# Kernel tuning notes

Measured on AMD Instinct MI355X. Metric: run time of the kernel, lower is better.

Reference implementation:

```python
import jax, jax.numpy as jnp
import numpy as np

NEG_SLOPE = 0.2  # PyG GATConv default
BN_EPS = 1e-5
NUM_GRAPHS = 128


def _bn(x, g, b, m, v):
    # eval-mode BatchNorm1d with running stats
    return (x - m) * jax.lax.rsqrt(v + BN_EPS) * g + b


def _gat_conv(x, src, dst, mask, W, a_src, a_dst, bias):
    # PyG GATConv: per-head linear, edge logits LeakyReLU(a_src.Wx_j + a_dst.Wx_i),
    # segment-softmax over incoming edges of each dst node, scatter-add messages.
    N = x.shape[0]
    H, C = a_src.shape
    xw = (x @ W).reshape(N, H, C)                       # [N,H,C]
    logit_s = (xw * a_src).sum(-1)                      # [N,H]
    logit_d = (xw * a_dst).sum(-1)                      # [N,H]
    e = jax.nn.leaky_relu(logit_s[src] + logit_d[dst], NEG_SLOPE)  # [E,H]
    e = jnp.where(mask[:, None], e, -1e30)              # edges filtered by edge_weights==1
    m = jax.ops.segment_max(e, dst, num_segments=N)     # [N,H]
    m = jnp.maximum(m, -1e30)                           # guard empty segments
    p = jnp.exp(e - m[dst]) * mask[:, None].astype(e.dtype)
    denom = jax.ops.segment_sum(p, dst, num_segments=N) + 1e-16
    alpha = p / denom[dst]                              # [E,H]
    out = jax.ops.segment_sum(xw[src] * alpha[..., None], dst, num_segments=N)
    return out.reshape(N, H * C) + bias


def setup_inputs() -> dict:
    key = jax.random.key(0)
    ks = jax.random.split(key, 20)
    N, E, F, G, NC = 20000, 320000, 128, NUM_GRAPHS, 10
    E0, E1, H = 256, 512, 2
    C = E1 // H

    def lin(k, fi, fo):
        return jax.random.normal(k, (fi, fo), jnp.float32) / np.float32(np.sqrt(fi))

    def bn(k, n):
        k1, k2, k3, k4 = jax.random.split(k, 4)
        g = 1.0 + 0.1 * jax.random.normal(k1, (n,), jnp.float32)
        b = 0.1 * jax.random.normal(k2, (n,), jnp.float32)
        m = 0.1 * jax.random.normal(k3, (n,), jnp.float32)
        v = 1.0 + 0.5 * jax.random.uniform(k4, (n,), jnp.float32)
        return g, b, m, v

    d = {}
    d['x'] = jax.random.normal(ks[0], (N, F), jnp.float32)
    d['edge_index'] = jax.random.randint(ks[1], (2, E), 0, N, dtype=jnp.int32)
    d['edge_weights'] = jnp.ones((E,), jnp.int32)
    d['batch'] = jnp.sort(jax.random.randint(ks[2], (N,), 0, G, dtype=jnp.int32))
    d['mlp_w1'] = lin(ks[3], F, E0); d['mlp_b1'] = jnp.zeros((E0,), jnp.float32)
    d['bn1_g'], d['bn1_b'], d['bn1_m'], d['bn1_v'] = bn(ks[4], E0)
    d['mlp_w2'] = lin(ks[5], E0, E0); d['mlp_b2'] = jnp.zeros((E0,), jnp.float32)
    d['bn2_g'], d['bn2_b'], d['bn2_m'], d['bn2_v'] = bn(ks[6], E0)
    d['gat0_w'] = lin(ks[7], E0, H * C)
    d['gat0_asrc'] = 0.1 * jax.random.normal(ks[8], (H, C), jnp.float32)
    d['gat0_adst'] = 0.1 * jax.random.normal(ks[9], (H, C), jnp.float32)
    d['gat0_bias'] = jnp.zeros((H * C,), jnp.float32)
    d['gat1_w'] = lin(ks[10], E1, H * C)
    d['gat1_asrc'] = 0.1 * jax.random.normal(ks[11], (H, C), jnp.float32)
    d['gat1_adst'] = 0.1 * jax.random.normal(ks[12], (H, C), jnp.float32)
    d['gat1_bias'] = jnp.zeros((H * C,), jnp.float32)
    d['bn3_g'], d['bn3_b'], d['bn3_m'], d['bn3_v'] = bn(ks[13], E1)
    d['fin_w1'] = lin(ks[14], E1, E1); d['fin_b1'] = jnp.zeros((E1,), jnp.float32)
    d['fin_w2'] = lin(ks[15], E1, NC); d['fin_b2'] = jnp.zeros((NC,), jnp.float32)
    return d


def reference(x, edge_index, edge_weights, batch,
              mlp_w1, mlp_b1, bn1_g, bn1_b, bn1_m, bn1_v,
              mlp_w2, mlp_b2, bn2_g, bn2_b, bn2_m, bn2_v,
              gat0_w, gat0_asrc, gat0_adst, gat0_bias,
              gat1_w, gat1_asrc, gat1_adst, gat1_bias,
              bn3_g, bn3_b, bn3_m, bn3_v,
              fin_w1, fin_b1, fin_w2, fin_b2):
    src, dst = edge_index[0], edge_index[1]
    mask = edge_weights == 1
    # initial MLP (dropout is identity in eval)
    h = jax.nn.relu(_bn(x @ mlp_w1 + mlp_b1, bn1_g, bn1_b, bn1_m, bn1_v))
    h = jax.nn.relu(_bn(h @ mlp_w2 + mlp_b2, bn2_g, bn2_b, bn2_m, bn2_v))
    # GAT layers
    h = _gat_conv(h, src, dst, mask, gat0_w, gat0_asrc, gat0_adst, gat0_bias)
    h = _gat_conv(h, src, dst, mask, gat1_w, gat1_asrc, gat1_adst, gat1_bias)
    # global mean pool over graphs
    sums = jax.ops.segment_sum(h, batch, num_segments=NUM_GRAPHS)
    cnt = jax.ops.segment_sum(jnp.ones((h.shape[0], 1), h.dtype), batch, num_segments=NUM_GRAPHS)
    pooled = sums / jnp.maximum(cnt, 1.0)
    # final head: BN -> ReLU -> Linear -> ReLU -> Linear
    z = jax.nn.relu(_bn(pooled, bn3_g, bn3_b, bn3_m, bn3_v))
    z = jax.nn.relu(z @ fin_w1 + fin_b1)
    return z @ fin_w2 + fin_b2
```

## Files before the change

kernel.cpp:

```cpp
#include <hip/hip_runtime.h>

typedef unsigned short u16;

constexpr int NN = 20000;
constexpr int EE = 320000;
constexpr int FD = 128;
constexpr int C0 = 256;
constexpr int C1 = 512;
constexpr int NG = 128;
constexpr int NC = 10;
constexpr int NBLK = (NN + 255) / 256;
constexpr int HB  = 320;
constexpr int EST = HB * 256;
constexpr int LGB = 640;
constexpr int PSPL = 16;

constexpr size_t OFF_XB   = 0;
constexpr size_t OFF_H1   = OFF_XB  + (size_t)NN * FD * 2;
constexpr size_t OFF_H2   = OFF_H1  + (size_t)NN * C0 * 2;
constexpr size_t OFF_XW   = OFF_H2  + (size_t)NN * C0 * 2;
constexpr size_t OFF_H34  = OFF_XW  + (size_t)NN * C1 * 2;
constexpr size_t OFF_LS   = OFF_H34 + (size_t)NN * C1 * 2;
constexpr size_t OFF_LD   = OFF_LS  + (size_t)NN * 2 * 4;
constexpr size_t OFF_DEG  = OFF_LD  + (size_t)NN * 2 * 4;
constexpr size_t OFF_OFFS = OFF_DEG + (size_t)NN * 4;
constexpr size_t OFF_CUR  = OFF_OFFS + 80016;
constexpr size_t OFF_CSRC = OFF_CUR + (size_t)NN * 4;
constexpr size_t OFF_GCNT = OFF_CSRC + (size_t)EE * 4;
constexpr size_t OFF_GOFF = OFF_GCNT + 512;
constexpr size_t OFF_PART = OFF_GOFF + 768;
constexpr size_t OFF_PTOT = OFF_PART + 512;
constexpr size_t OFF_Z1   = OFF_PTOT + 256;
constexpr size_t OFF_Z2   = OFF_Z1  + (size_t)NG * C1 * 2;
constexpr size_t OFF_ST   = OFF_Z2  + (size_t)NG * C1 * 2;
constexpr size_t OFF_W1T  = OFF_ST  + 8192;
constexpr size_t OFF_W2T  = OFF_W1T + (size_t)FD * C0 * 2;
constexpr size_t OFF_G0T  = OFF_W2T + (size_t)C0 * C0 * 2;
constexpr size_t OFF_G1T  = OFF_G0T + (size_t)C0 * C1 * 2;
constexpr size_t OFF_AUX  = OFF_G1T + (size_t)C1 * C1 * 2;
constexpr size_t OFF_FLAG = OFF_AUX  + 0;
constexpr size_t OFF_A0S  = OFF_AUX  + 256;
constexpr size_t OFF_A0D  = OFF_AUX  + 1280;
constexpr size_t OFF_A1S  = OFF_AUX  + 2304;
constexpr size_t OFF_A1D  = OFF_AUX  + 3328;
constexpr size_t OFF_GB0  = OFF_AUX  + 4352;
constexpr size_t OFF_GB1  = OFF_AUX  + 6400;
constexpr size_t OFF_FB1  = OFF_AUX  + 8448;
constexpr size_t OFF_FB2  = OFF_AUX  + 10496;
constexpr size_t OFF_GMX  = OFF_AUX  + 10752;
constexpr size_t OFF_PP   = OFF_AUX  + 11008;
constexpr size_t OFF_DENA = OFF_PP + (size_t)NG * PSPL * C1 * 4;
constexpr size_t OFF_P0   = OFF_XB;
constexpr size_t OFF_P1   = OFF_XB + (size_t)EE * 4;

__device__ inline float bf2f(u16 u) { return __uint_as_float(((unsigned)u) << 16); }
__device__ inline u16 f2bf(float f) {
    unsigned u = __float_as_uint(f);
    unsigned r = u + 0x7fffu + ((u >> 16) & 1u);
    return (u16)(r >> 16);
}
__device__ inline float ldf(const void* p, long i, unsigned f) {
    return f ? ((const float*)p)[i] : bf2f(((const u16*)p)[i]);
}
__device__ inline unsigned encf(float f) {
    unsigned u = __float_as_uint(f);
    return (u & 0x80000000u) ? ~u : (u | 0x80000000u);
}
__device__ inline float decf(unsigned e) {
    return (e & 0x80000000u) ? __uint_as_float(e ^ 0x80000000u) : __uint_as_float(~e);
}
__device__ inline void unpack8(uint4 r, float* v) {
    v[0] = __uint_as_float(r.x << 16); v[1] = __uint_as_float(r.x & 0xffff0000u);
    v[2] = __uint_as_float(r.y << 16); v[3] = __uint_as_float(r.y & 0xffff0000u);
    v[4] = __uint_as_float(r.z << 16); v[5] = __uint_as_float(r.z & 0xffff0000u);
    v[6] = __uint_as_float(r.w << 16); v[7] = __uint_as_float(r.w & 0xffff0000u);
}

typedef __bf16 bf16x8_t __attribute__((ext_vector_type(8)));
typedef float  f32x4_t  __attribute__((ext_vector_type(4)));

__device__ __forceinline__ void gl_lds16(const u16* g, u16* l) {
    __builtin_amdgcn_global_load_lds((const __attribute__((address_space(1))) void*)g,
                                     (__attribute__((address_space(3))) void*)l, 16, 0, 0);
}

__global__ void detect_dtype(const u16* __restrict__ x, const u16* __restrict__ w,
                             const u16* __restrict__ fw, unsigned* flag) {
    __shared__ int cnt;
    if (threadIdx.x == 0) cnt = 0;
    __syncthreads();
    int c = 0;
    for (int i = threadIdx.x; i < 4096; i += 256) {
        c += (((x[i]  >> 7) & 0xFF) == 0xFF);
        c += (((w[i]  >> 7) & 0xFF) == 0xFF);
        c += (((fw[i] >> 7) & 0xFF) == 0xFF);
    }
    atomicAdd(&cnt, c);
    __syncthreads();
    if (threadIdx.x == 0) *flag = (cnt >= 2) ? 1u : 0u;
}

__global__ void cvt_x(const unsigned* __restrict__ flag, const void* __restrict__ xin,
                      u16* __restrict__ XB, int* __restrict__ deg, int* __restrict__ gcnt,
                      unsigned* __restrict__ gmxu) {
    int i = blockIdx.x * 256 + threadIdx.x;
    if (i < NN) deg[i] = 0;
    if (i < NG) gcnt[i] = 0;
    if (i < 4)  gmxu[i] = encf(-1e30f);
    if (*flag) {
        float4 v = ((const float4*)xin)[i];
        ushort4 r;
        r.x = f2bf(v.x); r.y = f2bf(v.y); r.z = f2bf(v.z); r.w = f2bf(v.w);
        ((ushort4*)XB)[i] = r;
    } else {
        ((ushort4*)XB)[i] = ((const ushort4*)xin)[i];
    }
}

__global__ __launch_bounds__(512) void prep_trans(const unsigned* __restrict__ flag,
                            const void* g1, const void* b1, const void* m1, const void* v1, const void* lb1,
                            const void* g2, const void* b2, const void* m2, const void* v2, const void* lb2,
                            const void* g3, const void* b3, const void* m3, const void* v3,
                            const void* a0s, const void* a0d, const void* gb0in,
                            const void* a1s, const void* a1d, const void* gb1in,
                            const void* fb1in, const void* fb2in,
                            float* S1, float* T1, float* S2, float* T2, float* S3, float* T3,
                            u16* A0S, u16* A0D, u16* A1S, u16* A1D,
                            float* GB0, float* GB1, float* FB1, float* FB2,
                            const void* w1, const void* w2, const void* g0w, const void* g1w,
                            u16* w1T, u16* w2T, u16* g0T, u16* g1T) {
    unsigned f = *flag;
    if (blockIdx.x == 0) {
        int c = threadIdx.x;
        if (c < 256) {
            float s = ldf(g1, c, f) / sqrtf(ldf(v1, c, f) + 1e-5f);
            S1[c] = s; T1[c] = s * (ldf(lb1, c, f) - ldf(m1, c, f)) + ldf(b1, c, f);
            float s2 = ldf(g2, c, f) / sqrtf(ldf(v2, c, f) + 1e-5f);
            S2[c] = s2; T2[c] = s2 * (ldf(lb2, c, f) - ldf(m2, c, f)) + ldf(b2, c, f);
        }
        float s3 = ldf(g3, c, f) / sqrtf(ldf(v3, c, f) + 1e-5f);
        S3[c] = s3; T3[c] = ldf(b3, c, f) - ldf(m3, c, f) * s3;
        A0S[c] = f2bf(ldf(a0s, c, f));
        A0D[c] = f2bf(ldf(a0d, c, f));
        A1S[c] = f2bf(ldf(a1s, c, f));
        A1D[c] = f2bf(ldf(a1d, c, f));
        GB0[c] = ldf(gb0in, c, f);
        GB1[c] = ldf(gb1in, c, f);
        FB1[c] = ldf(fb1in, c, f);
        if (c < NC) FB2[c] = ldf(fb2in, c, f);
        return;
    }
    int b = blockIdx.x - 1;
    const void* B; u16* BT; int K, logN, base;
    if (b < 64)       { B = w1;  BT = w1T; K = FD; logN = 8; base = 0; }
    else if (b < 192) { B = w2;  BT = w2T; K = C0; logN = 8; base = 64; }
    else if (b < 448) { B = g0w; BT = g0T; K = C0; logN = 9; base = 192; }
    else              { B = g1w; BT = g1T; K = C1; logN = 9; base = 448; }
    int idx = (b - base) * 512 + threadIdx.x;
    int N = 1 << logN;
    int k = idx >> logN, n = idx & (N - 1);
    u16 v = f ? f2bf(((const float*)B)[idx]) : ((const u16*)B)[idx];
    BT[(size_t)n * K + k] = v;
}

__global__ __launch_bounds__(256) void hist_k(const int* __restrict__ dst, const int* __restrict__ ew,
                                              const int* __restrict__ batch,
                                              int* __restrict__ deg, int* __restrict__ gcnt) {
    int tid = blockIdx.x * 256 + threadIdx.x;
    int lane = threadIdx.x & 63;
#pragma unroll
    for (int j = 0; j < 4; j++) {
        int e = tid + j * EST;
        if (e < EE && ew[e] == 1) atomicAdd(&deg[dst[e]], 1);
    }
    int n = tid;
    if (n < NN) {
        int g = batch[n];
        int pg = __shfl_up(g, 1);
        bool head = (lane == 0) || (pg != g);
        unsigned long long act = __ballot(1);
        unsigned long long hm  = __ballot(head);
        if (head) {
            unsigned long long above = (lane < 63) ? ((hm >> (lane + 1)) << (lane + 1)) : 0ull;
            int limit = 64 - __builtin_clzll(act);
            int nxt = above ? __builtin_ctzll(above) : limit;
            atomicAdd(&gcnt[g], nxt - lane);
        }
    }
}
__global__ __launch_bounds__(256) void scan_blk(const int* __restrict__ deg, int* __restrict__ off,
                                                int* __restrict__ part) {
    __shared__ int tmp[256];
    int tid = threadIdx.x, i = blockIdx.x * 256 + tid;
    int v = (i < NN) ? deg[i] : 0;
    tmp[tid] = v;
    __syncthreads();
#pragma unroll
    for (int s = 1; s < 256; s <<= 1) {
        int a = (tid >= s) ? tmp[tid - s] : 0;
        __syncthreads();
        if (tid >= s) tmp[tid] += a;
        __syncthreads();
    }
    if (i < NN) off[i] = tmp[tid] - v;
    if (tid == 255) part[blockIdx.x] = tmp[255];
}
__global__ __launch_bounds__(128) void scan_small(int* __restrict__ part, int* __restrict__ ptot,
                                                  const int* __restrict__ gcnt, int* __restrict__ goff) {
    __shared__ int tmp[128];
    int tid = threadIdx.x;
    int v = (tid < NBLK) ? part[tid] : 0;
    tmp[tid] = v;
    __syncthreads();
#pragma unroll
    for (int s = 1; s < 128; s <<= 1) {
        int a = (tid >= s) ? tmp[tid - s] : 0;
        __syncthreads();
        if (tid >= s) tmp[tid] += a;
        __syncthreads();
    }
    if (tid < NBLK) part[tid] = tmp[tid] - v;
    if (tid == 127) *ptot = tmp[127];
    __syncthreads();
    int g = gcnt[tid];
    tmp[tid] = g;
    __syncthreads();
#pragma unroll
    for (int s = 1; s < 128; s <<= 1) {
        int a = (tid >= s) ? tmp[tid - s] : 0;
        __syncthreads();
        if (tid >= s) tmp[tid] += a;
        __syncthreads();
    }
    goff[tid] = tmp[tid] - g;
    if (tid == 127) goff[128] = tmp[127];
}
__global__ __launch_bounds__(256) void scan_add(int* __restrict__ off, const int* __restrict__ part,
                                                const int* __restrict__ ptot, int* __restrict__ cursor) {
    int tid = threadIdx.x, i = blockIdx.x * 256 + tid;
    if (i < NN) {
        int o = off[i] + part[blockIdx.x];
        off[i] = o;
        cursor[i] = o;
    }
    if (i == 0) off[NN] = *ptot;
}
__global__ __launch_bounds__(256) void csr_fill(const int* __restrict__ src, const int* __restrict__ dst,
                                                const int* __restrict__ ew,
                                                int* __restrict__ cursor, u16* __restrict__ csrc) {
    int tid = blockIdx.x * 256 + threadIdx.x;
    bool ok[4]; int sv[4]; int p[4];
#pragma unroll
    for (int j = 0; j < 4; j++) {
        int e = tid + j * EST;
        ok[j] = false; sv[j] = 0; p[j] = 0;
        if (e < EE && ew[e] == 1) {
            ok[j] = true;
            sv[j] = src[e];
            p[j] = atomicAdd(&cursor[dst[e]], 1);
        }
    }
#pragma unroll
    for (int j = 0; j < 4; j++) if (ok[j]) csrc[p[j]] = (u16)sv[j];
}

template <int EPI>
__global__ __launch_bounds__(256) void gemm_tile(const u16* __restrict__ A, const u16* __restrict__ BT,
                                                 u16* __restrict__ Cm,
                                                 const float* __restrict__ S, const float* __restrict__ T,
                                                 int M, int N, int K) {
    __shared__ u16 As[128 * 32];
    __shared__ u16 Bs[128 * 32];
    const int tid  = threadIdx.x;
    const int wave = tid >> 6;
    const int lane = tid & 63;
    const int quad = lane >> 4;
    const int l16  = lane & 15;
    const int wr0  = (wave >> 1) * 64;
    const int wc0  = (wave & 1) * 64;
    const int row0 = blockIdx.x * 128;
    const int col0 = blockIdx.y * 128;

    const int lr = lane >> 2;
    const int lk = (lane & 3) * 8;
    int r0l = wave * 32 + lr;
    int r1l = r0l + 16;
    int gr0 = row0 + r0l; if (gr0 >= M) gr0 = M - 1;
    int gr1 = row0 + r1l; if (gr1 >= M) gr1 = M - 1;
    const u16* ga0 = A  + (size_t)gr0 * K + lk;
    const u16* ga1 = A  + (size_t)gr1 * K + lk;
    const u16* gb0 = BT + (size_t)(col0 + r0l) * K + lk;
    const u16* gb1 = BT + (size_t)(col0 + r1l) * K + lk;
    u16* la0 = As + (size_t)(wave * 32)      * 32 + lane * 8;
    u16* la1 = As + (size_t)(wave * 32 + 16) * 32 + lane * 8;
    u16* lb0 = Bs + (size_t)(wave * 32)      * 32 + lane * 8;
    u16* lb1 = Bs + (size_t)(wave * 32 + 16) * 32 + lane * 8;

    f32x4_t acc[4][4];
#pragma unroll
    for (int r = 0; r < 4; r++)
#pragma unroll
        for (int c = 0; c < 4; c++)
#pragma unroll
            for (int i = 0; i < 4; i++) acc[r][c][i] = 0.f;

    for (int k0 = 0; k0 < K; k0 += 32) {
        gl_lds16(ga0 + k0, la0);
        gl_lds16(ga1 + k0, la1);
        gl_lds16(gb0 + k0, lb0);
        gl_lds16(gb1 + k0, lb1);
        __syncthreads();

        bf16x8_t a[4], b[4];
#pragma unroll
        for (int r = 0; r < 4; r++)
            a[r] = *(const bf16x8_t*)(As + (size_t)(wr0 + r * 16 + l16) * 32 + quad * 8);
#pragma unroll
        for (int c = 0; c < 4; c++)
            b[c] = *(const bf16x8_t*)(Bs + (size_t)(wc0 + c * 16 + l16) * 32 + quad * 8);
#pragma unroll
        for (int r = 0; r < 4; r++)
#pragma unroll
            for (int c = 0; c < 4; c++)
                acc[r][c] = __builtin_amdgcn_mfma_f32_16x16x32_bf16(a[r], b[c], acc[r][c], 0, 0, 0);
        __syncthreads();
    }

#pragma unroll
    for (int r = 0; r < 4; r++) {
        int rb = row0 + wr0 + r * 16 + quad * 4;
#pragma unroll
        for (int c = 0; c < 4; c++) {
            int col = col0 + wc0 + c * 16 + l16;
            float sc = (EPI == 1) ? S[col] : 0.f;
            float sh = (EPI == 1) ? T[col] : 0.f;
#pragma unroll
            for (int i = 0; i < 4; i++) {
                int row = rb + i;
                if (row < M) {
                    float v = acc[r][c][i];
                    if (EPI == 1) v = fmaxf(v * sc + sh, 0.f);
                    Cm[(size_t)row * N + col] = f2bf(v);
                }
            }
        }
    }
}

__global__ __launch_bounds__(256) void gat_logits(const u16* __restrict__ xw, const u16* __restrict__ asrc,
                                                  const u16* __restrict__ adst, float* __restrict__ ls,
                                                  float* __restrict__ ld, unsigned* __restrict__ gmx) {
    __shared__ float smax[8];
    int lane = threadIdx.x & 63;
    int wv   = threadIdx.x >> 6;
    int h    = lane >> 5;
    uint4 av = ((const uint4*)asrc)[lane];
    uint4 dv = ((const uint4*)adst)[lane];
    float a[8], d[8];
    unpack8(av, a); unpack8(dv, d);
    float mm = -1e30f;
    int n = blockIdx.x * 4 + wv;
    uint4 xv;
    if (n < NN) xv = ((const uint4*)(xw + (size_t)n * C1))[lane];
    while (n < NN) {
        int n2 = n + LGB * 4;
        uint4 nx;
        if (n2 < NN) nx = ((const uint4*)(xw + (size_t)n2 * C1))[lane];
        float x[8];
        unpack8(xv, x);
        float ps = 0.f, pd = 0.f;
#pragma unroll
        for (int j = 0; j < 8; j++) { ps += x[j] * a[j]; pd += x[j] * d[j]; }
#pragma unroll
        for (int m = 16; m >= 1; m >>= 1) { ps += __shfl_xor(ps, m); pd += __shfl_xor(pd, m); }
        if ((lane & 31) == 0) {
            ls[n * 2 + h] = ps;
            ld[n * 2 + h] = pd;
        }
        mm = fmaxf(mm, ps);
        xv = nx; n = n2;
    }
    if ((lane & 31) == 0) smax[wv * 2 + h] = mm;
    __syncthreads();
    if (threadIdx.x < 2) {
        float m = fmaxf(fmaxf(smax[threadIdx.x], smax[2 + threadIdx.x]),
                        fmaxf(smax[4 + threadIdx.x], smax[6 + threadIdx.x]));
        atomicMax(&gmx[threadIdx.x], encf(m));
    }
}

__global__ __launch_bounds__(256) void gat_prep(const int* __restrict__ off, const u16* __restrict__ csrc,
                                                const float* __restrict__ ls, const float* __restrict__ ld,
                                                const unsigned* __restrict__ gmx,
                                                float* __restrict__ P0, float* __restrict__ P1,
                                                float* __restrict__ denA) {
    int n = blockIdx.x * 4 + (threadIdx.x >> 6);
    if (n >= NN) return;
    int lane = threadIdx.x & 63;
    int h = lane >> 5;
    int el = lane & 31;
    int beg = off[n], end = off[n + 1];
    float2 ldv = ((const float2*)ld)[n];
    float ldh = h ? ldv.y : ldv.x;
    float gm = decf(gmx[h]) + ldh;
    float mhat = gm > 0.f ? gm : 0.2f * gm;
    float* __restrict__ Ph = h ? P1 : P0;
    float den = 0.f;
    for (int base = beg; base < end; base += 32) {
        int e = base + el;
        int ec = e < end ? e : end - 1;
        int sv = csrc[ec];
        float vv = ls[sv * 2 + h] + ldh;
        vv = vv > 0.f ? vv : 0.2f * vv;
        float p = __expf(vv - mhat);
        float pm = (e < end) ? p : 0.f;
#pragma unroll
        for (int m = 16; m >= 1; m >>= 1) pm += __shfl_xor(pm, m);
        den += pm;
        if (e < end) Ph[e] = p;
    }
    if (el == 0) denA[n * 2 + h] = den;
}

__device__ __forceinline__ void proc_edge(uint4 c, float w, float* acc) {
    float x[8];
    unpack8(c, x);
#pragma unroll
    for (int q = 0; q < 8; q++) acc[q] = fmaf(w, x[q], acc[q]);
}

__global__ __launch_bounds__(256) void gat_aggregate(const int* __restrict__ off, const u16* __restrict__ csrc,
                                                     const float* __restrict__ P0, const float* __restrict__ P1,
                                                     const float* __restrict__ denA,
                                                     const u16* __restrict__ xw,
                                                     const float* __restrict__ bias, u16* __restrict__ outh) {
    int n = blockIdx.x * 4 + (threadIdx.x >> 6);
    if (n >= NN) return;
    const int lane = threadIdx.x & 63;
    const int h    = lane >> 5;
    const int el   = lane & 31;
    const int hoff = h << 5;
    const float* __restrict__ Ph = h ? P1 : P0;
    int beg = off[n], end = off[n + 1];

    float acc[8];
#pragma unroll
    for (int q = 0; q < 8; q++) acc[q] = 0.f;

#define ROWLD(S) (((const uint4*)(xw + (size_t)(S) * C1))[lane])

    for (int base = beg; base < end; base += 32) {
        int cnt = end - base; if (cnt > 32) cnt = 32;
        int e = base + el;
        int ec = e < end ? e : end - 1;
        int sv = csrc[ec];
        float pv = Ph[ec];

        uint4 r0 = ROWLD(__shfl(sv, 0));
        uint4 r1 = ROWLD(__shfl(sv, 1));
        uint4 r2 = ROWLD(__shfl(sv, 2));
        uint4 r3 = ROWLD(__shfl(sv, 3));

        for (int j = 0; j < cnt; j += 4) {
            uint4 c0 = r0, c1 = r1, c2 = r2, c3 = r3;
            float w0 = __shfl(pv, j + hoff);
            float w1 = __shfl(pv, j + 1 + hoff);
            float w2 = __shfl(pv, j + 2 + hoff);
            float w3 = __shfl(pv, j + 3 + hoff);
            if (j + 4 < cnt) {
                r0 = ROWLD(__shfl(sv, j + 4));
                r1 = ROWLD(__shfl(sv, j + 5));
                r2 = ROWLD(__shfl(sv, j + 6));
                r3 = ROWLD(__shfl(sv, j + 7));
            }
            proc_edge(c0, w0, acc);
            if (j + 1 < cnt) proc_edge(c1, w1, acc);
            if (j + 2 < cnt) proc_edge(c2, w2, acc);
            if (j + 3 < cnt) proc_edge(c3, w3, acc);
        }
    }
#undef ROWLD

    float inv = 1.f / fmaxf(denA[n * 2 + h], 1e-30f);
    int cb = lane * 8;
    const float4* bp = (const float4*)(bias + cb);
    float4 b0 = bp[0], b1 = bp[1];
    uint4 st;
    st.x = (unsigned)f2bf(fmaf(acc[0], inv, b0.x)) | ((unsigned)f2bf(fmaf(acc[1], inv, b0.y)) << 16);
    st.y = (unsigned)f2bf(fmaf(acc[2], inv, b0.z)) | ((unsigned)f2bf(fmaf(acc[3], inv, b0.w)) << 16);
    st.z = (unsigned)f2bf(fmaf(acc[4], inv, b1.x)) | ((unsigned)f2bf(fmaf(acc[5], inv, b1.y)) << 16);
    st.w = (unsigned)f2bf(fmaf(acc[6], inv, b1.z)) | ((unsigned)f2bf(fmaf(acc[7], inv, b1.w)) << 16);
    ((uint4*)(outh + (size_t)n * C1 + cb))[0] = st;
}

__global__ __launch_bounds__(128) void pool_part(const u16* __restrict__ h4, const int* __restrict__ goff,
                                                 float* __restrict__ pp) {
    int g = blockIdx.x, s = blockIdx.y, t = threadIdx.x;
    int b = goff[g], e = goff[g + 1];
    int len = e - b;
    int chunk = (len + PSPL - 1) / PSPL;
    int n0 = b + s * chunk;
    int n1 = n0 + chunk; if (n1 > e) n1 = e;
    float s0 = 0.f, s1 = 0.f, s2 = 0.f, s3 = 0.f;
    for (int n = n0; n < n1; n++) {
        ushort4 v = *(const ushort4*)(h4 + (size_t)n * C1 + t * 4);
        s0 += bf2f(v.x); s1 += bf2f(v.y); s2 += bf2f(v.z); s3 += bf2f(v.w);
    }
    float4* dst = (float4*)(pp + ((size_t)g * PSPL + s) * C1 + t * 4);
    *dst = make_float4(s0, s1, s2, s3);
}

__global__ __launch_bounds__(512) void head_all(const unsigned* __restrict__ flag,
                                                const float* __restrict__ pp, const int* __restrict__ goff,
                                                const float* __restrict__ S3, const float* __restrict__ T3,
                                                const void* __restrict__ w1, const float* __restrict__ FB1,
                                                const void* __restrict__ w2, const float* __restrict__ FB2,
                                                void* __restrict__ out) {
    __shared__ float zrow[512];
    __shared__ float z2row[512];
    __shared__ float red[512];
    int g = blockIdx.x, t = threadIdx.x;
    unsigned f = *flag;
    float s = 0.f;
#pragma unroll
    for (int k = 0; k < PSPL; k++) s += pp[((size_t)g * PSPL + k) * C1 + t];
    int b = goff[g], e = goff[g + 1];
    float mean = s / fmaxf((float)(e - b), 1.f);
    float v = fmaxf(mean * S3[t] + T3[t], 0.f);
    zrow[t] = bf2f(f2bf(v));
    __syncthreads();
    float acc = 0.f;
    if (f) {
        const float* w = (const float*)w1;
        for (int k = 0; k < 512; k++) acc = fmaf(zrow[k], w[(size_t)k * 512 + t], acc);
    } else {
        const u16* w = (const u16*)w1;
        for (int k = 0; k < 512; k++) acc = fmaf(zrow[k], bf2f(w[(size_t)k * 512 + t]), acc);
    }
    acc += FB1[t];
    z2row[t] = bf2f(f2bf(fmaxf(acc, 0.f)));
    __syncthreads();
    float z2t = z2row[t];
    for (int o = 0; o < NC; o++) {
        float p = f ? z2t * ((const float*)w2)[(size_t)t * NC + o]
                    : z2t * bf2f(((const u16*)w2)[(size_t)t * NC + o]);
        red[t] = p;
        __syncthreads();
#pragma unroll
        for (int sd = 256; sd >= 1; sd >>= 1) {
            if (t < sd) red[t] += red[t + sd];
            __syncthreads();
        }
        if (t == 0) {
            float vv = red[0] + FB2[o];
            if (f) ((float*)out)[g * NC + o] = vv;
            else   ((u16*)out)[g * NC + o] = f2bf(vv);
        }
        __syncthreads();
    }
}

extern "C" void kernel_launch(void* const* d_in, const int* in_sizes, int n_in,
                              void* d_out, int out_size, void* d_ws, size_t ws_size,
                              hipStream_t stream) {
    (void)in_sizes; (void)n_in; (void)out_size; (void)ws_size;

    const void* x      = d_in[0];
    const int* ei      = (const int*)d_in[1];
    const int* src     = ei;
    const int* dst     = ei + EE;
    const int* ew      = (const int*)d_in[2];
    const int* batch   = (const int*)d_in[3];
    const void* mlp_w1 = d_in[4];
    const void* mlp_b1 = d_in[5];
    const void *bn1g = d_in[6], *bn1b = d_in[7], *bn1m = d_in[8], *bn1v = d_in[9];
    const void* mlp_w2 = d_in[10];
    const void* mlp_b2 = d_in[11];
    const void *bn2g = d_in[12], *bn2b = d_in[13], *bn2m = d_in[14], *bn2v = d_in[15];
    const void* g0w    = d_in[16];
    const void* g0as   = d_in[17];
    const void* g0ad   = d_in[18];
    const void* g0bias = d_in[19];
    const void* g1w    = d_in[20];
    const void* g1as   = d_in[21];
    const void* g1ad   = d_in[22];
    const void* g1bias = d_in[23];
    const void *bn3g = d_in[24], *bn3b = d_in[25], *bn3m = d_in[26], *bn3v = d_in[27];
    const void* fin_w1 = d_in[28];
    const void* fin_b1 = d_in[29];
    const void* fin_w2 = d_in[30];
    const void* fin_b2 = d_in[31];

    char* ws = (char*)d_ws;
    u16*  XB   = (u16*)(ws + OFF_XB);
    u16*  h1   = (u16*)(ws + OFF_H1);
    u16*  h2   = (u16*)(ws + OFF_H2);
    u16*  xw   = (u16*)(ws + OFF_XW);
    u16*  h34  = (u16*)(ws + OFF_H34);
    float* ls  = (float*)(ws + OFF_LS);
    float* ld  = (float*)(ws + OFF_LD);
    int*  deg  = (int*)(ws + OFF_DEG);
    int*  off  = (int*)(ws + OFF_OFFS);
    int*  cur  = (int*)(ws + OFF_CUR);
    u16*  csrc = (u16*)(ws + OFF_CSRC);
    int*  gcnt = (int*)(ws + OFF_GCNT);
    int*  goff = (int*)(ws + OFF_GOFF);
    int*  part = (int*)(ws + OFF_PART);
    int*  ptot = (int*)(ws + OFF_PTOT);
    float* S1 = (float*)(ws + OFF_ST);
    float* T1 = S1 + 256;
    float* S2 = T1 + 256;
    float* T2 = S2 + 256;
    float* S3 = T2 + 256;
    float* T3 = S3 + 512;
    u16* w1T = (u16*)(ws + OFF_W1T);
    u16* w2T = (u16*)(ws + OFF_W2T);
    u16* g0T = (u16*)(ws + OFF_G0T);
    u16* g1T = (u16*)(ws + OFF_G1T);
    unsigned* flag = (unsigned*)(ws + OFF_FLAG);
    u16* A0S = (u16*)(ws + OFF_A0S);
    u16* A0D = (u16*)(ws + OFF_A0D);
    u16* A1S = (u16*)(ws + OFF_A1S);
    u16* A1D = (u16*)(ws + OFF_A1D);
    float* GB0 = (float*)(ws + OFF_GB0);
    float* GB1 = (float*)(ws + OFF_GB1);
    float* FB1 = (float*)(ws + OFF_FB1);
    float* FB2 = (float*)(ws + OFF_FB2);
    unsigned* GMXU = (unsigned*)(ws + OFF_GMX);
    float* PP = (float*)(ws + OFF_PP);
    float* DENA = (float*)(ws + OFF_DENA);
    float* P0 = (float*)(ws + OFF_P0);
    float* P1 = (float*)(ws + OFF_P1);

    detect_dtype<<<1, 256, 0, stream>>>((const u16*)x, (const u16*)mlp_w1, (const u16*)fin_w1, flag);
    cvt_x<<<(NN * FD / 4) / 256, 256, 0, stream>>>(flag, x, XB, deg, gcnt, GMXU);
    prep_trans<<<961, 512, 0, stream>>>(flag,
                                        bn1g, bn1b, bn1m, bn1v, mlp_b1,
                                        bn2g, bn2b, bn2m, bn2v, mlp_b2,
                                        bn3g, bn3b, bn3m, bn3v,
                                        g0as, g0ad, g0bias, g1as, g1ad, g1bias,
                                        fin_b1, fin_b2,
                                        S1, T1, S2, T2, S3, T3,
                                        A0S, A0D, A1S, A1D, GB0, GB1, FB1, FB2,
                                        mlp_w1, mlp_w2, g0w, g1w, w1T, w2T, g0T, g1T);

    hist_k<<<HB, 256, 0, stream>>>(dst, ew, batch, deg, gcnt);
    scan_blk<<<NBLK, 256, 0, stream>>>(deg, off, part);
    scan_small<<<1, 128, 0, stream>>>(part, ptot, gcnt, goff);
    scan_add<<<NBLK, 256, 0, stream>>>(off, part, ptot, cur);
    csr_fill<<<HB, 256, 0, stream>>>(src, dst, ew, cur, csrc);

    gemm_tile<1><<<dim3(157, 2), 256, 0, stream>>>(XB, w1T, h1, S1, T1, NN, C0, FD);
    gemm_tile<1><<<dim3(157, 2), 256, 0, stream>>>(h1, w2T, h2, S2, T2, NN, C0, C0);

    gemm_tile<0><<<dim3(157, 4), 256, 0, stream>>>(h2, g0T, xw, nullptr, nullptr, NN, C1, C0);
    gat_logits<<<LGB, 256, 0, stream>>>(xw, A0S, A0D, ls, ld, GMXU);
    gat_prep<<<NN / 4, 256, 0, stream>>>(off, csrc, ls, ld, GMXU, P0, P1, DENA);
    gat_aggregate<<<NN / 4, 256, 0, stream>>>(off, csrc, P0, P1, DENA, xw, GB0, h34);

    gemm_tile<0><<<dim3(157, 4), 256, 0, stream>>>(h34, g1T, xw, nullptr, nullptr, NN, C1, C1);
    gat_logits<<<LGB, 256, 0, stream>>>(xw, A1S, A1D, ls, ld, GMXU + 2);
    gat_prep<<<NN / 4, 256, 0, stream>>>(off, csrc, ls, ld, GMXU + 2, P0, P1, DENA);
    gat_aggregate<<<NN / 4, 256, 0, stream>>>(off, csrc, P0, P1, DENA, xw, GB1, h34);

    pool_part<<<dim3(NG, PSPL), 128, 0, stream>>>(h34, goff, PP);
    head_all<<<NG, 512, 0, stream>>>(flag, PP, goff, S3, T3, fin_w1, FB1, fin_w2, FB2, d_out);
}
```

Before: 405.7 us.

## Fuse GAT logit dot-products into GEMM epilogue and use exact per-node max

The attention logit projections (xw·a_src, xw·a_dst) are now computed in the GEMM epilogue from the rounded outputs. Partial sums per column tile go to a buffer, and a small ls_combine kernel adds them. This removes the separate gat_logits pass that re-read xw, and it drops the global-max atomic and its init. gat_prep now makes an extra pass over each node's edges to compute the exact per-segment max instead of a global upper bound. Separately, the GEMM K-step doubles to 64 with an XOR-swizzled LDS layout, which means fewer barriers but more shared memory per block.

```diff
diff --git a/kernel.cpp b/kernel.cpp
--- a/kernel.cpp
+++ b/kernel.cpp
@@ -12,7 +12,6 @@
 constexpr int NBLK = (NN + 255) / 256;
 constexpr int HB  = 320;
 constexpr int EST = HB * 256;
-constexpr int LGB = 640;
 constexpr int PSPL = 16;
 
 constexpr size_t OFF_XB   = 0;
@@ -47,9 +46,9 @@
 constexpr size_t OFF_GB1  = OFF_AUX  + 6400;
 constexpr size_t OFF_FB1  = OFF_AUX  + 8448;
 constexpr size_t OFF_FB2  = OFF_AUX  + 10496;
-constexpr size_t OFF_GMX  = OFF_AUX  + 10752;
 constexpr size_t OFF_PP   = OFF_AUX  + 11008;
 constexpr size_t OFF_DENA = OFF_PP + (size_t)NG * PSPL * C1 * 4;
+constexpr size_t OFF_PLS  = OFF_DENA + (size_t)NN * 2 * 4;
 constexpr size_t OFF_P0   = OFF_XB;
 constexpr size_t OFF_P1   = OFF_XB + (size_t)EE * 4;
 
@@ -62,13 +61,6 @@
 __device__ inline float ldf(const void* p, long i, unsigned f) {
     return f ? ((const float*)p)[i] : bf2f(((const u16*)p)[i]);
 }
-__device__ inline unsigned encf(float f) {
-    unsigned u = __float_as_uint(f);
-    return (u & 0x80000000u) ? ~u : (u | 0x80000000u);
-}
-__device__ inline float decf(unsigned e) {
-    return (e & 0x80000000u) ? __uint_as_float(e ^ 0x80000000u) : __uint_as_float(~e);
-}
 __device__ inline void unpack8(uint4 r, float* v) {
     v[0] = __uint_as_float(r.x << 16); v[1] = __uint_as_float(r.x & 0xffff0000u);
     v[2] = __uint_as_float(r.y << 16); v[3] = __uint_as_float(r.y & 0xffff0000u);
@@ -101,12 +93,10 @@
 }
 
 __global__ void cvt_x(const unsigned* __restrict__ flag, const void* __restrict__ xin,
-                      u16* __restrict__ XB, int* __restrict__ deg, int* __restrict__ gcnt,
-                      unsigned* __restrict__ gmxu) {
+                      u16* __restrict__ XB, int* __restrict__ deg, int* __restrict__ gcnt) {
     int i = blockIdx.x * 256 + threadIdx.x;
     if (i < NN) deg[i] = 0;
     if (i < NG) gcnt[i] = 0;
-    if (i < 4)  gmxu[i] = encf(-1e30f);
     if (*flag) {
         float4 v = ((const float4*)xin)[i];
         ushort4 r;
@@ -268,9 +258,11 @@
 __global__ __launch_bounds__(256) void gemm_tile(const u16* __restrict__ A, const u16* __restrict__ BT,
                                                  u16* __restrict__ Cm,
                                                  const float* __restrict__ S, const float* __restrict__ T,
+                                                 const u16* __restrict__ asrc, const u16* __restrict__ adst,
+                                                 float2* __restrict__ pls,
                                                  int M, int N, int K) {
-    __shared__ u16 As[128 * 32];
-    __shared__ u16 Bs[128 * 32];
+    __shared__ u16 As[128 * 64];
+    __shared__ u16 Bs[128 * 64];
     const int tid  = threadIdx.x;
     const int wave = tid >> 6;
     const int lane = tid & 63;
@@ -281,20 +273,18 @@
     const int row0 = blockIdx.x * 128;
     const int col0 = blockIdx.y * 128;
 
-    const int lr = lane >> 2;
-    const int lk = (lane & 3) * 8;
-    int r0l = wave * 32 + lr;
-    int r1l = r0l + 16;
-    int gr0 = row0 + r0l; if (gr0 >= M) gr0 = M - 1;
-    int gr1 = row0 + r1l; if (gr1 >= M) gr1 = M - 1;
-    const u16* ga0 = A  + (size_t)gr0 * K + lk;
-    const u16* ga1 = A  + (size_t)gr1 * K + lk;
-    const u16* gb0 = BT + (size_t)(col0 + r0l) * K + lk;
-    const u16* gb1 = BT + (size_t)(col0 + r1l) * K + lk;
-    u16* la0 = As + (size_t)(wave * 32)      * 32 + lane * 8;
-    u16* la1 = As + (size_t)(wave * 32 + 16) * 32 + lane * 8;
-    u16* lb0 = Bs + (size_t)(wave * 32)      * 32 + lane * 8;
-    u16* lb1 = Bs + (size_t)(wave * 32 + 16) * 32 + lane * 8;
+    const int srow = lane >> 3;
+    const int sk   = ((lane & 7) ^ srow) * 8;
+    const u16* gaP[4]; const u16* gbP[4]; u16* laP[4]; u16* lbP[4];
+#pragma unroll
+    for (int i = 0; i < 4; i++) {
+        int rl = wave * 32 + i * 8 + srow;
+        int gr = row0 + rl; if (gr >= M) gr = M - 1;
+        gaP[i] = A  + (size_t)gr * K + sk;
+        gbP[i] = BT + (size_t)(col0 + rl) * K + sk;
+        laP[i] = As + (size_t)rl * 64 + (lane & 7) * 8;
+        lbP[i] = Bs + (size_t)rl * 64 + (lane & 7) * 8;
+    }
 
     f32x4_t acc[4][4];
 #pragma unroll
@@ -304,94 +294,107 @@
 #pragma unroll
             for (int i = 0; i < 4; i++) acc[r][c][i] = 0.f;
 
-    for (int k0 = 0; k0 < K; k0 += 32) {
-        gl_lds16(ga0 + k0, la0);
-        gl_lds16(ga1 + k0, la1);
-        gl_lds16(gb0 + k0, lb0);
-        gl_lds16(gb1 + k0, lb1);
-        __syncthreads();
-
-        bf16x8_t a[4], b[4];
-#pragma unroll
-        for (int r = 0; r < 4; r++)
-            a[r] = *(const bf16x8_t*)(As + (size_t)(wr0 + r * 16 + l16) * 32 + quad * 8);
-#pragma unroll
-        for (int c = 0; c < 4; c++)
-            b[c] = *(const bf16x8_t*)(Bs + (size_t)(wc0 + c * 16 + l16) * 32 + quad * 8);
-#pragma unroll
-        for (int r = 0; r < 4; r++)
-#pragma unroll
-            for (int c = 0; c < 4; c++)
-                acc[r][c] = __builtin_amdgcn_mfma_f32_16x16x32_bf16(a[r], b[c], acc[r][c], 0, 0, 0);
-        __syncthreads();
-    }
-
+    for (int k0 = 0; k0 < K; k0 += 64) {
+#pragma unroll
+        for (int i = 0; i < 4; i++) {
+            gl_lds16(gaP[i] + k0, laP[i]);
+            gl_lds16(gbP[i] + k0, lbP[i]);
+        }
+        __syncthreads();
+
+#pragma unroll
+        for (int kk = 0; kk < 2; kk++) {
+            bf16x8_t a[4], b[4];
+#pragma unroll
+            for (int r = 0; r < 4; r++) {
+                int rr = wr0 + r * 16 + l16;
+                a[r] = *(const bf16x8_t*)(As + (size_t)rr * 64 + (((kk * 4 + quad) ^ (rr & 7)) * 8));
+            }
+#pragma unroll
+            for (int c = 0; c < 4; c++) {
+                int cc = wc0 + c * 16 + l16;
+                b[c] = *(const bf16x8_t*)(Bs + (size_t)cc * 64 + (((kk * 4 + quad) ^ (cc & 7)) * 8));
+            }
+#pragma unroll
+            for (int r = 0; r < 4; r++)
+#pragma unroll
+                for (int c = 0; c < 4; c++)
+                    acc[r][c] = __builtin_amdgcn_mfma_f32_16x16x32_bf16(a[r], b[c], acc[r][c], 0, 0, 0);
+        }
+        __syncthreads();
+    }
+
+    float2* lred = reinterpret_cast<float2*>(As);
 #pragma unroll
     for (int r = 0; r < 4; r++) {
         int rb = row0 + wr0 + r * 16 + quad * 4;
+        float ps[4] = {0.f, 0.f, 0.f, 0.f}, pd[4] = {0.f, 0.f, 0.f, 0.f};
 #pragma unroll
         for (int c = 0; c < 4; c++) {
             int col = col0 + wc0 + c * 16 + l16;
             float sc = (EPI == 1) ? S[col] : 0.f;
             float sh = (EPI == 1) ? T[col] : 0.f;
+            float av_ = 0.f, dv_ = 0.f;
+            if (EPI == 3) { av_ = bf2f(asrc[col]); dv_ = bf2f(adst[col]); }
 #pragma unroll
             for (int i = 0; i < 4; i++) {
                 int row = rb + i;
-                if (row < M) {
-                    float v = acc[r][c][i];
-                    if (EPI == 1) v = fmaxf(v * sc + sh, 0.f);
-                    Cm[(size_t)row * N + col] = f2bf(v);
+                float v = acc[r][c][i];
+                if (EPI == 1) v = fmaxf(v * sc + sh, 0.f);
+                u16 bv = f2bf(v);
+                if (row < M) Cm[(size_t)row * N + col] = bv;
+                if (EPI == 3) {
+                    float vb = bf2f(bv);
+                    ps[i] = fmaf(vb, av_, ps[i]);
+                    pd[i] = fmaf(vb, dv_, pd[i]);
                 }
             }
         }
-    }
-}
-
-__global__ __launch_bounds__(256) void gat_logits(const u16* __restrict__ xw, const u16* __restrict__ asrc,
-                                                  const u16* __restrict__ adst, float* __restrict__ ls,
-                                                  float* __restrict__ ld, unsigned* __restrict__ gmx) {
-    __shared__ float smax[8];
-    int lane = threadIdx.x & 63;
-    int wv   = threadIdx.x >> 6;
-    int h    = lane >> 5;
-    uint4 av = ((const uint4*)asrc)[lane];
-    uint4 dv = ((const uint4*)adst)[lane];
-    float a[8], d[8];
-    unpack8(av, a); unpack8(dv, d);
-    float mm = -1e30f;
-    int n = blockIdx.x * 4 + wv;
-    uint4 xv;
-    if (n < NN) xv = ((const uint4*)(xw + (size_t)n * C1))[lane];
-    while (n < NN) {
-        int n2 = n + LGB * 4;
-        uint4 nx;
-        if (n2 < NN) nx = ((const uint4*)(xw + (size_t)n2 * C1))[lane];
-        float x[8];
-        unpack8(xv, x);
-        float ps = 0.f, pd = 0.f;
-#pragma unroll
-        for (int j = 0; j < 8; j++) { ps += x[j] * a[j]; pd += x[j] * d[j]; }
-#pragma unroll
-        for (int m = 16; m >= 1; m >>= 1) { ps += __shfl_xor(ps, m); pd += __shfl_xor(pd, m); }
-        if ((lane & 31) == 0) {
-            ls[n * 2 + h] = ps;
-            ld[n * 2 + h] = pd;
-        }
-        mm = fmaxf(mm, ps);
-        xv = nx; n = n2;
-    }
-    if ((lane & 31) == 0) smax[wv * 2 + h] = mm;
-    __syncthreads();
-    if (threadIdx.x < 2) {
-        float m = fmaxf(fmaxf(smax[threadIdx.x], smax[2 + threadIdx.x]),
-                        fmaxf(smax[4 + threadIdx.x], smax[6 + threadIdx.x]));
-        atomicMax(&gmx[threadIdx.x], encf(m));
+        if (EPI == 3) {
+#pragma unroll
+            for (int i = 0; i < 4; i++) {
+#pragma unroll
+                for (int m = 1; m <= 8; m <<= 1) {
+                    ps[i] += __shfl_xor(ps[i], m);
+                    pd[i] += __shfl_xor(pd[i], m);
+                }
+            }
+            if (l16 == 0) {
+#pragma unroll
+                for (int i = 0; i < 4; i++) {
+                    int rl = wr0 + r * 16 + quad * 4 + i;
+                    lred[(size_t)(wave & 1) * 128 + rl] = make_float2(ps[i], pd[i]);
+                }
+            }
+        }
+    }
+    if (EPI == 3) {
+        __syncthreads();
+        if (tid < 128) {
+            int row = row0 + tid;
+            if (row < M) {
+                float2 a0 = lred[tid], a1 = lred[128 + tid];
+                pls[(size_t)blockIdx.y * NN + row] = make_float2(a0.x + a1.x, a0.y + a1.y);
+            }
+        }
+    }
+}
+
+__global__ __launch_bounds__(256) void ls_combine(const float2* __restrict__ pls,
+                                                  float* __restrict__ ls, float* __restrict__ ld) {
+    int n = blockIdx.x * 256 + threadIdx.x;
+    if (n >= NN) return;
+#pragma unroll
+    for (int h = 0; h < 2; h++) {
+        float2 a = pls[(size_t)(2 * h) * NN + n];
+        float2 b = pls[(size_t)(2 * h + 1) * NN + n];
+        ls[n * 2 + h] = a.x + b.x;
+        ld[n * 2 + h] = a.y + b.y;
     }
 }
 
 __global__ __launch_bounds__(256) void gat_prep(const int* __restrict__ off, const u16* __restrict__ csrc,
                                                 const float* __restrict__ ls, const float* __restrict__ ld,
-                                                const unsigned* __restrict__ gmx,
                                                 float* __restrict__ P0, float* __restrict__ P1,
                                                 float* __restrict__ denA) {
     int n = blockIdx.x * 4 + (threadIdx.x >> 6);
@@ -402,9 +405,19 @@
     int beg = off[n], end = off[n + 1];
     float2 ldv = ((const float2*)ld)[n];
     float ldh = h ? ldv.y : ldv.x;
-    float gm = decf(gmx[h]) + ldh;
-    float mhat = gm > 0.f ? gm : 0.2f * gm;
     float* __restrict__ Ph = h ? P1 : P0;
+    float vmax = -1e30f;
+    for (int base = beg; base < end; base += 32) {
+        int e = base + el;
+        int ec = e < end ? e : end - 1;
+        int sv = csrc[ec];
+        float vv = ls[sv * 2 + h] + ldh;
+        vv = vv > 0.f ? vv : 0.2f * vv;
+        if (e < end) vmax = fmaxf(vmax, vv);
+    }
+#pragma unroll
+    for (int m = 16; m >= 1; m >>= 1) vmax = fmaxf(vmax, __shfl_xor(vmax, m));
+    float mhat = vmax;
     float den = 0.f;
     for (int base = beg; base < end; base += 32) {
         int e = base + el;
@@ -626,14 +639,14 @@
     float* GB1 = (float*)(ws + OFF_GB1);
     float* FB1 = (float*)(ws + OFF_FB1);
     float* FB2 = (float*)(ws + OFF_FB2);
-    unsigned* GMXU = (unsigned*)(ws + OFF_GMX);
     float* PP = (float*)(ws + OFF_PP);
     float* DENA = (float*)(ws + OFF_DENA);
+    float2* PLS = (float2*)(ws + OFF_PLS);
     float* P0 = (float*)(ws + OFF_P0);
     float* P1 = (float*)(ws + OFF_P1);
 
     detect_dtype<<<1, 256, 0, stream>>>((const u16*)x, (const u16*)mlp_w1, (const u16*)fin_w1, flag);
-    cvt_x<<<(NN * FD / 4) / 256, 256, 0, stream>>>(flag, x, XB, deg, gcnt, GMXU);
+    cvt_x<<<(NN * FD / 4) / 256, 256, 0, stream>>>(flag, x, XB, deg, gcnt);
     prep_trans<<<961, 512, 0, stream>>>(flag,
                                         bn1g, bn1b, bn1m, bn1v, mlp_b1,
                                         bn2g, bn2b, bn2m, bn2v, mlp_b2,
@@ -650,17 +663,17 @@
     scan_add<<<NBLK, 256, 0, stream>>>(off, part, ptot, cur);
     csr_fill<<<HB, 256, 0, stream>>>(src, dst, ew, cur, csrc);
 
-    gemm_tile<1><<<dim3(157, 2), 256, 0, stream>>>(XB, w1T, h1, S1, T1, NN, C0, FD);
-    gemm_tile<1><<<dim3(157, 2), 256, 0, stream>>>(h1, w2T, h2, S2, T2, NN, C0, C0);
-
-    gemm_tile<0><<<dim3(157, 4), 256, 0, stream>>>(h2, g0T, xw, nullptr, nullptr, NN, C1, C0);
-    gat_logits<<<LGB, 256, 0, stream>>>(xw, A0S, A0D, ls, ld, GMXU);
-    gat_prep<<<NN / 4, 256, 0, stream>>>(off, csrc, ls, ld, GMXU, P0, P1, DENA);
+    gemm_tile<1><<<dim3(157, 2), 256, 0, stream>>>(XB, w1T, h1, S1, T1, nullptr, nullptr, nullptr, NN, C0, FD);
+    gemm_tile<1><<<dim3(157, 2), 256, 0, stream>>>(h1, w2T, h2, S2, T2, nullptr, nullptr, nullptr, NN, C0, C0);
+
+    gemm_tile<3><<<dim3(157, 4), 256, 0, stream>>>(h2, g0T, xw, nullptr, nullptr, A0S, A0D, PLS, NN, C1, C0);
+    ls_combine<<<NBLK, 256, 0, stream>>>(PLS, ls, ld);
+    gat_prep<<<NN / 4, 256, 0, stream>>>(off, csrc, ls, ld, P0, P1, DENA);
     gat_aggregate<<<NN / 4, 256, 0, stream>>>(off, csrc, P0, P1, DENA, xw, GB0, h34);
 
-    gemm_tile<0><<<dim3(157, 4), 256, 0, stream>>>(h34, g1T, xw, nullptr, nullptr, NN, C1, C1);
-    gat_logits<<<LGB, 256, 0, stream>>>(xw, A1S, A1D, ls, ld, GMXU + 2);
-    gat_prep<<<NN / 4, 256, 0, stream>>>(off, csrc, ls, ld, GMXU + 2, P0, P1, DENA);
+    gemm_tile<3><<<dim3(157, 4), 256, 0, stream>>>(h34, g1T, xw, nullptr, nullptr, A1S, A1D, PLS, NN, C1, C1);
+    ls_combine<<<NBLK, 256, 0, stream>>>(PLS, ls, ld);
+    gat_prep<<<NN / 4, 256, 0, stream>>>(off, csrc, ls, ld, P0, P1, DENA);
     gat_aggregate<<<NN / 4, 256, 0, stream>>>(off, csrc, P0, P1, DENA, xw, GB1, h34);
 
     pool_part<<<dim3(NG, PSPL), 128, 0, stream>>>(h34, goff, PP);
```

Measured after the change: 380.7 us. 6.2% less time.
